# Performance work log

Measured on AMD Instinct MI355X. Metric: run time of the kernel, lower is better.

The kernel has to match this reference:

```python
import jax, jax.numpy as jnp
import numpy as np

B, L, D, N = 2, 8192, 1024, 512
EPS = 1e-5


def setup_inputs() -> dict:
    key = jax.random.key(0)
    ks = jax.random.split(key, 6)
    x = jax.random.normal(ks[0], (B, L, D), dtype=jnp.float32)
    Lambda_real = jax.random.normal(ks[1], (N,), dtype=jnp.float32)
    Lambda_imag = jax.random.normal(ks[2], (N,), dtype=jnp.float32)
    C_real = jax.random.normal(ks[3], (D, N), dtype=jnp.float32)
    C_imag = jax.random.normal(ks[4], (D, N), dtype=jnp.float32)
    param_D = jax.random.normal(ks[5], (D,), dtype=jnp.float32)
    gamma = jnp.ones((D,), dtype=jnp.float32)   # LayerNorm weight
    beta = jnp.zeros((D,), dtype=jnp.float32)   # LayerNorm bias
    return {"x": x, "Lambda_real": Lambda_real, "Lambda_imag": Lambda_imag,
            "C_real": C_real, "C_imag": C_imag, "param_D": param_D,
            "gamma": gamma, "beta": beta}


def reference(x, Lambda_real, Lambda_imag, C_real, C_imag, param_D, gamma, beta):
    seq_len = x.shape[1]
    # LayerNorm over last dim (biased variance, eps=1e-5, elementwise affine)
    mean = jnp.mean(x, axis=-1, keepdims=True)
    var = jnp.mean(jnp.square(x - mean), axis=-1, keepdims=True)
    u = (x - mean) * jax.lax.rsqrt(var + EPS) * gamma + beta   # [b, l, d]
    residual = u * param_D                                      # [b, l, d]
    # Diagonal SSM kernel synthesis
    Lam = -jnp.exp(Lambda_real) + 1j * jnp.exp(Lambda_imag)     # [n] complex
    C = (C_real + 1j * C_imag) * (jnp.exp(Lam) - 1.0) / Lam     # [d, n]
    ar = jnp.arange(seq_len, dtype=jnp.float32)
    S = jnp.exp(Lam[:, None] * ar[None, :])                     # [n, l] Vandermonde-like
    K = jnp.einsum('hn,nl->lh', C, S).real                      # [l, d]
    # FFT long convolution (linear conv via 2L zero-padding)
    n_fft = seq_len * 2
    u_f = jnp.fft.rfft(u, n=n_fft, axis=-2)                     # [b, l+1, d]
    K_f = jnp.fft.rfft(K, n=n_fft, axis=-2)                     # [l+1, d]
    y = jnp.fft.irfft(u_f * K_f, n=n_fft, axis=-2)[..., :seq_len, :]
    return y + residual
```

## Files before the change

### kernel.cpp

```cpp
#include <hip/hip_runtime.h>
#include <math.h>

#define LLEN 8192
#define DDIM 1024
#define NB   2
#define NMODE 512
#define MFFT 8192
#define SLEN 4096
#define KF_STRIDE 8208

#define PIDX(i) ((i) + ((i) >> 4))
#define FBUF 8704

#define OFF_UT   ((size_t)0)
#define OFF_KF   ((size_t)67108864)
#define OFF_KT   ((size_t)134348800)
#define OFF_CPK  ((size_t)167903232)
#define OFF_MEAN ((size_t)172097536)
#define OFF_RSTD ((size_t)172163072)
#define OFF_LAMR ((size_t)172228608)
#define OFF_LAMID ((size_t)172230656)
#define OFF_WR   ((size_t)172234752)
#define OFF_WI   ((size_t)172236800)
#define OFF_CUT  ((size_t)172238848)
#define OFF_TW   ((size_t)172240896)
#define OFF_TWR  ((size_t)172306432)
#define OFF_SORTN ((size_t)172371976)
#define OFF_TCNT  ((size_t)172374024)
#define WS_NEED  ((size_t)172374088)

#define OFF_SP   OFF_KF

__global__ __launch_bounds__(256) void ln_stats_kernel(const float* __restrict__ x,
                                                       float* __restrict__ mean,
                                                       float* __restrict__ rstd) {
  __shared__ float red[16];
  int row = blockIdx.x;
  int tid = threadIdx.x;
  const float4* xr = (const float4*)(x + (size_t)row * DDIM);
  float4 v = xr[tid];
  float s = v.x + v.y + v.z + v.w;
  float q = v.x*v.x + v.y*v.y + v.z*v.z + v.w*v.w;
  #pragma unroll
  for (int off = 32; off; off >>= 1) { s += __shfl_down(s, off); q += __shfl_down(q, off); }
  int wid = tid >> 6;
  if ((tid & 63) == 0) { red[wid] = s; red[8 + wid] = q; }
  __syncthreads();
  if (tid == 0) {
    float ts = red[0] + red[1] + red[2] + red[3];
    float tq = red[8] + red[9] + red[10] + red[11];
    float m = ts * (1.0f / DDIM);
    float var = tq * (1.0f / DDIM) - m * m;
    mean[row] = m;
    rstd[row] = rsqrtf(var + 1e-5f);
  }
}

__global__ __launch_bounds__(256) void transpose_ln_kernel(const float* __restrict__ x,
                                                           const float* __restrict__ mean,
                                                           const float* __restrict__ rstd,
                                                           const float* __restrict__ gamma,
                                                           const float* __restrict__ beta,
                                                           float* __restrict__ uT) {
  __shared__ float tile[32][33];
  int lt = blockIdx.x * 32, dt = blockIdx.y * 32, b = blockIdx.z;
  int c = threadIdx.x & 31, r0 = threadIdx.x >> 5;
  float gv = gamma[dt + c], bv = beta[dt + c];
  #pragma unroll
  for (int i = 0; i < 4; i++) {
    int r = r0 + i * 8;
    float m = mean[(size_t)b * LLEN + lt + r];
    float rs = rstd[(size_t)b * LLEN + lt + r];
    float xv = x[((size_t)b * LLEN + lt + r) * DDIM + dt + c];
    tile[r][c] = (xv - m) * rs * gv + bv;
  }
  __syncthreads();
  #pragma unroll
  for (int i = 0; i < 4; i++) {
    int r = r0 + i * 8;
    uT[((size_t)b * DDIM + dt + r) * LLEN + lt + c] = tile[c][r];
  }
}

__global__ void build_tables_kernel(const float* __restrict__ Lr, const float* __restrict__ Li,
                                    float* lamr, double* lamid, float* wre, float* wim, int* cut,
                                    float2* twH, float2* twR) {
  int gid = blockIdx.x * 256 + threadIdx.x;
  if (gid < NMODE) {
    double lr = (double)Lr[gid], li = (double)Li[gid];
    double ar = -exp(lr);
    double ai = exp(li);
    lamr[gid] = (float)ar;
    lamid[gid] = ai;
    double em = exp(ar);
    double cs = cos(ai), sn = sin(ai);
    double er = em * cs - 1.0;
    double ei = em * sn;
    double den = ar * ar + ai * ai;
    wre[gid] = (float)((er * ar + ei * ai) / den);
    wim[gid] = (float)((ei * ar - er * ai) / den);
    int co = (int)(40.0 / (-ar)) + 1;
    cut[gid] = co > SLEN ? SLEN : co;
  }
  int j = gid - NMODE;
  if (j >= 0 && j < 8192) {
    if (j == 0) {
      twH[0] = make_float2(1.f, 0.f);
    } else {
      int lev = 31 - __clz(j);
      int Ls = 1 << lev;
      int p = j - Ls;
      double a = 3.14159265358979323846264338 * (double)p / (double)Ls;
      twH[j] = make_float2((float)cos(a), (float)sin(a));
    }
  }
  int k = gid - (NMODE + 8192);
  if (k >= 0 && k <= 8192) {
    double a = 6.283185307179586476925287 * (double)k / 16384.0;
    twR[k] = make_float2((float)cos(a), (float)sin(a));
  }
}

#define KB4_LT 256
#define NTILE (SLEN / KB4_LT)
__global__ __launch_bounds__(NMODE) void sortmodes_kernel(const int* __restrict__ cut,
                                                          int* __restrict__ sortn,
                                                          int* __restrict__ tcount) {
  __shared__ int sc[NMODE];
  int tid = threadIdx.x;
  sc[tid] = cut[tid];
  __syncthreads();
  int c = sc[tid];
  int rank = 0;
  for (int m = 0; m < NMODE; ++m) {
    int cm = sc[m];
    rank += (cm > c) || (cm == c && m < tid);
  }
  sortn[rank] = tid;
  if (tid < NTILE) {
    int l0 = tid * KB4_LT;
    int cnt = 0;
    for (int m = 0; m < NMODE; ++m) cnt += (sc[m] > l0);
    tcount[tid] = cnt;
  }
}

__global__ __launch_bounds__(256) void cpack_kernel(const float* __restrict__ Cr,
                                                    const float* __restrict__ Ci,
                                                    const float* __restrict__ wre,
                                                    const float* __restrict__ wim,
                                                    const int* __restrict__ sortn,
                                                    float2* __restrict__ Cpk) {
  int idx = blockIdx.x * 256 + threadIdx.x;
  int r = idx >> 10, d = idx & (DDIM - 1);
  int n = sortn[r];
  float cr = Cr[(size_t)d * NMODE + n], ci = Ci[(size_t)d * NMODE + n];
  float wr = wre[n], wi = wim[n];
  Cpk[idx] = make_float2(cr * wr - ci * wi, cr * wi + ci * wr);
}

__global__ __launch_bounds__(256) void sbuild_kernel(const float* __restrict__ lamr,
                                                     const double* __restrict__ lamid,
                                                     const int* __restrict__ cut,
                                                     const int* __restrict__ sortn,
                                                     float2* __restrict__ Spack) {
  int r = blockIdx.y;
  int n = sortn[r];
  int l = blockIdx.x * 256 + threadIdx.x;
  float sr = 0.f, si = 0.f;
  if (l < cut[n]) {
    float mag = expf(lamr[n] * (float)l);
    double ph = lamid[n] * (double)l;
    const double tp = 6.283185307179586476925287;
    const double itp = 1.0 / 6.283185307179586476925287;
    ph -= floor(ph * itp) * tp;
    float cs, sn; sincosf((float)ph, &sn, &cs);
    sr = mag * cs; si = mag * sn;
  }
  Spack[(size_t)r * SLEN + l] = make_float2(sr, si);
}

#define KB5_DT 4
__global__ __launch_bounds__(256) void kbuild7_kernel(const float2* __restrict__ Spack,
                                                      const float2* __restrict__ Cpk,
                                                      const int* __restrict__ tcount,
                                                      float* __restrict__ KT) {
  __shared__ float2 sC[NMODE][KB5_DT];
  int t = blockIdx.y;
  int d0 = blockIdx.x * KB5_DT;
  int tid = threadIdx.x;
  int nact = tcount[t];
  for (int i = tid; i < nact * KB5_DT; i += 256) {
    int r = i >> 2, dd = i & 3;
    sC[r][dd] = Cpk[(size_t)r * DDIM + d0 + dd];
  }
  __syncthreads();
  int l = t * KB4_LT + tid;
  float acc0 = 0.f, acc1 = 0.f, acc2 = 0.f, acc3 = 0.f;
  const float2* sp = Spack + l;
  int i = 0;
  int n8 = nact & ~7;
  for (; i < n8; i += 8) {
    const float2* p = sp + (size_t)i * SLEN;
    float2 s0 = p[0];
    float2 s1 = p[(size_t)1 * SLEN];
    float2 s2 = p[(size_t)2 * SLEN];
    float2 s3 = p[(size_t)3 * SLEN];
    float2 s4 = p[(size_t)4 * SLEN];
    float2 s5 = p[(size_t)5 * SLEN];
    float2 s6 = p[(size_t)6 * SLEN];
    float2 s7 = p[(size_t)7 * SLEN];
    #define KACC(ss, rr) { \
      float2 c0 = sC[rr][0], c1 = sC[rr][1], c2 = sC[rr][2], c3 = sC[rr][3]; \
      acc0 += ss.x * c0.x - ss.y * c0.y; \
      acc1 += ss.x * c1.x - ss.y * c1.y; \
      acc2 += ss.x * c2.x - ss.y * c2.y; \
      acc3 += ss.x * c3.x - ss.y * c3.y; }
    KACC(s0, i + 0) KACC(s1, i + 1) KACC(s2, i + 2) KACC(s3, i + 3)
    KACC(s4, i + 4) KACC(s5, i + 5) KACC(s6, i + 6) KACC(s7, i + 7)
  }
  for (; i < nact; ++i) {
    float2 s0 = sp[(size_t)i * SLEN];
    KACC(s0, i)
  }
  #undef KACC
  KT[(size_t)(d0 + 0) * SLEN + l] = acc0;
  KT[(size_t)(d0 + 1) * SLEN + l] = acc1;
  KT[(size_t)(d0 + 2) * SLEN + l] = acc2;
  KT[(size_t)(d0 + 3) * SLEN + l] = acc3;
}

#define R4BLK(b0, b2, b1, b3, wa, wb, o0, o1, o2, o3) { \
  float war=(wa).x, wai=sign*(wa).y, wbr=(wb).x, wbi=sign*(wb).y; \
  float t1r_=war*(b2).x - wai*(b2).y, t1i_=war*(b2).y + wai*(b2).x; \
  float t3r_=war*(b3).x - wai*(b3).y, t3i_=war*(b3).y + wai*(b3).x; \
  float Ar=(b0).x+t1r_, Ai=(b0).y+t1i_, Cr=(b0).x-t1r_, Ci=(b0).y-t1i_; \
  float Br=(b1).x+t3r_, Bi=(b1).y+t3i_, Dr=(b1).x-t3r_, Di=(b1).y-t3i_; \
  float Er=wbr*Br-wbi*Bi, Ei=wbr*Bi+wbi*Br; \
  float Fr=wbr*Dr-wbi*Di, Fi=wbr*Di+wbi*Dr; \
  dst[PIDX(o0)]=make_float2(Ar+Er,Ai+Ei); \
  dst[PIDX(o1)]=make_float2(Cr-sign*Fi,Ci+sign*Fr); \
  dst[PIDX(o2)]=make_float2(Ar-Er,Ai-Ei); \
  dst[PIDX(o3)]=make_float2(Cr+sign*Fi,Ci-sign*Fr); }

__device__ __forceinline__ void r8_stage(const float2* src, float2* dst,
                                         const float2* __restrict__ twH,
                                         int tid, float sign, int s) {
  int L = 1 << s;
  int j = tid;
  int p = j & (L - 1);
  int q = j >> s;
  float2 x0 = src[PIDX(j)];
  float2 x1 = src[PIDX(j + 1024)];
  float2 x2 = src[PIDX(j + 2048)];
  float2 x3 = src[PIDX(j + 3072)];
  float2 x4 = src[PIDX(j + 4096)];
  float2 x5 = src[PIDX(j + 5120)];
  float2 x6 = src[PIDX(j + 6144)];
  float2 x7 = src[PIDX(j + 7168)];
  float2 w1 = twH[L + p];
  float w1r = w1.x, w1i = sign * w1.y;
  float t4r = w1r*x4.x - w1i*x4.y, t4i = w1r*x4.y + w1i*x4.x;
  float t5r = w1r*x5.x - w1i*x5.y, t5i = w1r*x5.y + w1i*x5.x;
  float t6r = w1r*x6.x - w1i*x6.y, t6i = w1r*x6.y + w1i*x6.x;
  float t7r = w1r*x7.x - w1i*x7.y, t7i = w1r*x7.y + w1i*x7.x;
  float2 A0 = make_float2(x0.x + t4r, x0.y + t4i), B0 = make_float2(x0.x - t4r, x0.y - t4i);
  float2 A1 = make_float2(x1.x + t5r, x1.y + t5i), B1 = make_float2(x1.x - t5r, x1.y - t5i);
  float2 A2 = make_float2(x2.x + t6r, x2.y + t6i), B2 = make_float2(x2.x - t6r, x2.y - t6i);
  float2 A3 = make_float2(x3.x + t7r, x3.y + t7i), B3 = make_float2(x3.x - t7r, x3.y - t7i);
  int O = (q << (s + 3)) + p;
  R4BLK(A0, A2, A1, A3, twH[2*L + p], twH[4*L + p], O, O + 2*L, O + 4*L, O + 6*L)
  R4BLK(B0, B2, B1, B3, twH[3*L + p], twH[5*L + p], O + L, O + 3*L, O + 5*L, O + 7*L)
}

__device__ __forceinline__ void r8_first4(const float2* __restrict__ g, float2* dst,
                                          const float2* __restrict__ twH,
                                          int tid, float sign) {
  float2 x0 = g[tid];
  float2 x1 = g[tid + 1024];
  float2 x2 = g[tid + 2048];
  float2 x3 = g[tid + 3072];
  int O = tid << 3;
  R4BLK(x0, x2, x1, x3, twH[2], twH[4], O, O + 2, O + 4, O + 6)
  R4BLK(x0, x2, x1, x3, twH[3], twH[5], O + 1, O + 3, O + 5, O + 7)
}

__device__ __forceinline__ void r8_first2(const float2* __restrict__ g, float2* dst,
                                          const float2* __restrict__ twH,
                                          int tid, float sign) {
  float2 x0 = g[tid];
  float2 x1 = g[tid + 1024];
  float2 zf = make_float2(0.f, 0.f);
  int O = tid << 3;
  R4BLK(x0, zf, x1, zf, twH[2], twH[4], O, O + 2, O + 4, O + 6)
  R4BLK(x0, zf, x1, zf, twH[3], twH[5], O + 1, O + 3, O + 5, O + 7)
}

__device__ __forceinline__ void fwd_final_pair(const float2* sbuf, const float2* __restrict__ twH,
                                               int k, float2* zk, float2* zm) {
  float2 a1 = sbuf[PIDX(k)], b1 = sbuf[PIDX(k + 4096)];
  float2 w1 = twH[4096 + k];
  float br1 = w1.x*b1.x + w1.y*b1.y;
  float bi1 = w1.x*b1.y - w1.y*b1.x;
  *zk = make_float2(a1.x + br1, a1.y + bi1);
  float2 a2 = sbuf[PIDX(4096 - k)], b2 = sbuf[PIDX(8192 - k)];
  float2 w2 = twH[8192 - k];
  float br2 = w2.x*b2.x + w2.y*b2.y;
  float bi2 = w2.x*b2.y - w2.y*b2.x;
  *zm = make_float2(a2.x - br2, a2.y - bi2);
}

__global__ __launch_bounds__(1024) void kf_fft_kernel(const float* __restrict__ KT,
                                                      const float2* __restrict__ twH,
                                                      const float2* __restrict__ twR,
                                                      float2* __restrict__ Kf) {
  __shared__ float2 bufA[FBUF];
  __shared__ float2 bufB[FBUF];
  int d = blockIdx.x;
  int tid = threadIdx.x;
  const float2* row = (const float2*)(KT + (size_t)d * SLEN);
  const float sign = -1.f;
  { float2* dst = bufA; r8_first2(row, dst, twH, tid, sign); }
  __syncthreads();
  r8_stage(bufA, bufB, twH, tid, sign, 3);
  __syncthreads();
  r8_stage(bufB, bufA, twH, tid, sign, 6);
  __syncthreads();
  r8_stage(bufA, bufB, twH, tid, sign, 9);
  __syncthreads();
  const float scale = 1.0f / 8192.0f;
  float2* out = Kf + (size_t)d * KF_STRIDE;
  for (int k = tid; k <= 4096; k += 1024) {
    if (k == 0) {
      float2 s0 = bufB[PIDX(0)], s4 = bufB[PIDX(4096)];
      float2 z0 = make_float2(s0.x + s4.x, s0.y + s4.y);
      out[0]    = make_float2((z0.x + z0.y) * scale, 0.f);
      out[8192] = make_float2((z0.x - z0.y) * scale, 0.f);
    } else {
      float2 zk, zm;
      if (k == 4096) {
        float2 s0 = bufB[PIDX(0)], s4 = bufB[PIDX(4096)];
        zk = make_float2(s0.x - s4.x, s0.y - s4.y);
        zm = zk;
      } else {
        fwd_final_pair(bufB, twH, k, &zk, &zm);
      }
      float Ar = 0.5f * (zk.x + zm.x), Ai = 0.5f * (zk.y - zm.y);
      float Br = 0.5f * (zk.x - zm.x), Bi = 0.5f * (zk.y + zm.y);
      float2 t = twR[k];
      float c = t.x, sn = t.y;
      float e1r = sn * Br - c * Bi;
      float e1i = sn * Bi + c * Br;
      out[k]        = make_float2((Ar - e1r) * scale, (Ai - e1i) * scale);
      out[MFFT - k] = make_float2((Ar + e1r) * scale, (-Ai - e1i) * scale);
    }
  }
}

__global__ __launch_bounds__(1024) void conv_fft_kernel(float* __restrict__ uT,
                                                        const float2* __restrict__ twH,
                                                        const float2* __restrict__ twR,
                                                        const float2* __restrict__ Kf,
                                                        const float* __restrict__ pD) {
  __shared__ float2 bufA[FBUF];
  __shared__ float2 bufB[FBUF];
  int wg = blockIdx.x;
  int b = wg >> 10, d = wg & (DDIM - 1);
  int tid = threadIdx.x;
  float2* row = (float2*)(uT + ((size_t)b * DDIM + d) * LLEN);
  float sign = -1.f;
  { float2* dst = bufA; r8_first4(row, dst, twH, tid, sign); }
  __syncthreads();
  r8_stage(bufA, bufB, twH, tid, sign, 3);
  __syncthreads();
  r8_stage(bufB, bufA, twH, tid, sign, 6);
  __syncthreads();
  r8_stage(bufA, bufB, twH, tid, sign, 9);
  __syncthreads();
  const float2* kf = Kf + (size_t)d * KF_STRIDE;
  for (int k = tid; k <= 4096; k += 1024) {
    if (k == 0) {
      float2 s0 = bufB[PIDX(0)], s4 = bufB[PIDX(4096)];
      float2 z0 = make_float2(s0.x + s4.x, s0.y + s4.y);
      float U0 = z0.x + z0.y;
      float UM = z0.x - z0.y;
      float Y0 = U0 * kf[0].x;
      float YM = UM * kf[8192].x;
      bufA[PIDX(0)] = make_float2(0.5f * (Y0 + YM), 0.5f * (Y0 - YM));
    } else {
      float2 zk, zm;
      if (k == 4096) {
        float2 s0 = bufB[PIDX(0)], s4 = bufB[PIDX(4096)];
        zk = make_float2(s0.x - s4.x, s0.y - s4.y);
        zm = zk;
      } else {
        fwd_final_pair(bufB, twH, k, &zk, &zm);
      }
      float Ar = 0.5f * (zk.x + zm.x), Ai = 0.5f * (zk.y - zm.y);
      float Br = 0.5f * (zk.x - zm.x), Bi = 0.5f * (zk.y + zm.y);
      float2 t = twR[k];
      float c = t.x, sn = t.y;
      float e1r = sn * Br - c * Bi;
      float e1i = sn * Bi + c * Br;
      float Ukr = Ar - e1r, Uki = Ai - e1i;
      float Umr = Ar + e1r, Umi = -Ai - e1i;
      float2 kk = kf[k], km = kf[MFFT - k];
      float Ykr = Ukr * kk.x - Uki * kk.y, Yki = Ukr * kk.y + Uki * kk.x;
      float Ymr = Umr * km.x - Umi * km.y, Ymi = Umr * km.y + Umi * km.x;
      float Eyr = 0.5f * (Ykr + Ymr), Eyi = 0.5f * (Yki - Ymi);
      float Byr = 0.5f * (Ykr - Ymr), Byi = 0.5f * (Yki + Byi*0.f + Yki*0.f + Ymi);
      Byi = 0.5f * (Yki + Ymi);
      bufA[PIDX(k)]        = make_float2(Eyr - sn * Byr - c * Byi, Eyi + c * Byr - sn * Byi);
      bufA[PIDX(MFFT - k)] = make_float2(Eyr + sn * Byr + c * Byi, -Eyi + c * Byr - sn * Byi);
    }
  }
  __syncthreads();
  sign = +1.f;
  r8_stage(bufA, bufB, twH, tid, sign, 0);
  __syncthreads();
  r8_stage(bufB, bufA, twH, tid, sign, 3);
  __syncthreads();
  r8_stage(bufA, bufB, twH, tid, sign, 6);
  __syncthreads();
  r8_stage(bufB, bufA, twH, tid, sign, 9);
  __syncthreads();
  float pdv = pD[d];
  for (int j = tid; j < 4096; j += 1024) {
    float2 a = bufA[PIDX(j)];
    float2 bq = bufA[PIDX(j + 4096)];
    float2 w = twH[4096 + j];
    float br = w.x * bq.x - w.y * bq.y;
    float bi = w.x * bq.y + w.y * bq.x;
    float2 uv = row[j];
    row[j] = make_float2(a.x + br + uv.x * pdv, a.y + bi + uv.y * pdv);
  }
}

__global__ __launch_bounds__(256) void final_kernel(const float* __restrict__ yT,
                                                    float* __restrict__ out) {
  __shared__ float tile[32][33];
  int lt = blockIdx.x * 32, dt = blockIdx.y * 32, b = blockIdx.z;
  int c = threadIdx.x & 31, r0 = threadIdx.x >> 5;
  #pragma unroll
  for (int i = 0; i < 4; i++) {
    int r = r0 + i * 8;
    tile[r][c] = yT[((size_t)b * DDIM + dt + r) * LLEN + lt + c];
  }
  __syncthreads();
  #pragma unroll
  for (int i = 0; i < 4; i++) {
    int r = r0 + i * 8;
    out[((size_t)b * LLEN + lt + r) * DDIM + dt + c] = tile[c][r];
  }
}

extern "C" void kernel_launch(void* const* d_in, const int* in_sizes, int n_in,
                              void* d_out, int out_size, void* d_ws, size_t ws_size,
                              hipStream_t stream) {
  (void)in_sizes; (void)n_in; (void)out_size;
  if (ws_size < WS_NEED) return;
  const float* x     = (const float*)d_in[0];
  const float* Lr    = (const float*)d_in[1];
  const float* Li    = (const float*)d_in[2];
  const float* Cr    = (const float*)d_in[3];
  const float* Ci    = (const float*)d_in[4];
  const float* pD    = (const float*)d_in[5];
  const float* gamma = (const float*)d_in[6];
  const float* beta  = (const float*)d_in[7];
  float* out = (float*)d_out;
  char* ws = (char*)d_ws;

  float*  UT    = (float*)(ws + OFF_UT);
  float2* KF    = (float2*)(ws + OFF_KF);
  float2* SPK   = (float2*)(ws + OFF_SP);
  float*  KT    = (float*)(ws + OFF_KT);
  float2* CPK   = (float2*)(ws + OFF_CPK);
  float*  MEAN  = (float*)(ws + OFF_MEAN);
  float*  RSTD  = (float*)(ws + OFF_RSTD);
  float*  LAMR  = (float*)(ws + OFF_LAMR);
  double* LAMID = (double*)(ws + OFF_LAMID);
  float*  WRe   = (float*)(ws + OFF_WR);
  float*  WIm   = (float*)(ws + OFF_WI);
  int*    CUT   = (int*)(ws + OFF_CUT);
  float2* TWH   = (float2*)(ws + OFF_TW);
  float2* TWR   = (float2*)(ws + OFF_TWR);
  int*    SORTN = (int*)(ws + OFF_SORTN);
  int*    TCNT  = (int*)(ws + OFF_TCNT);

  ln_stats_kernel<<<NB * LLEN, 256, 0, stream>>>(x, MEAN, RSTD);
  transpose_ln_kernel<<<dim3(LLEN / 32, DDIM / 32, NB), 256, 0, stream>>>(x, MEAN, RSTD, gamma, beta, UT);
  build_tables_kernel<<<67, 256, 0, stream>>>(Lr, Li, LAMR, LAMID, WRe, WIm, CUT, TWH, TWR);
  sortmodes_kernel<<<1, NMODE, 0, stream>>>(CUT, SORTN, TCNT);
  cpack_kernel<<<(NMODE * DDIM) / 256, 256, 0, stream>>>(Cr, Ci, WRe, WIm, SORTN, CPK);
  sbuild_kernel<<<dim3(SLEN / 256, NMODE), 256, 0, stream>>>(LAMR, LAMID, CUT, SORTN, SPK);
  kbuild7_kernel<<<dim3(DDIM / KB5_DT, NTILE), 256, 0, stream>>>(SPK, CPK, TCNT, KT);
  kf_fft_kernel<<<DDIM, 1024, 0, stream>>>(KT, TWH, TWR, KF);
  conv_fft_kernel<<<NB * DDIM, 1024, 0, stream>>>(UT, TWH, TWR, KF, pD);
  final_kernel<<<dim3(LLEN / 32, DDIM / 32, NB), 256, 0, stream>>>(UT, out);
}
```

Before: 299.4 us.

## Make FFT stages in-place to halve LDS and allow two blocks per CU

Replaces the ping-pong shared buffers in the FFT kernels with a single buffer, putting a barrier between the loads and stores of each radix-8 stage. The pointwise spectrum multiply is also restructured so each thread computes its symmetric pairs in registers before writing back in place. This halves LDS use per block (about 70KB down to 35KB), so more 1024-thread blocks can be resident per CU, at the cost of an extra barrier per stage and more register pressure.

```diff
diff --git a/kernel.cpp b/kernel.cpp
--- a/kernel.cpp
+++ b/kernel.cpp
@@ -243,21 +243,20 @@
   dst[PIDX(o2)]=make_float2(Ar-Er,Ai-Ei); \
   dst[PIDX(o3)]=make_float2(Cr+sign*Fi,Ci-sign*Fr); }
 
-__device__ __forceinline__ void r8_stage(const float2* src, float2* dst,
-                                         const float2* __restrict__ twH,
-                                         int tid, float sign, int s) {
+__device__ __forceinline__ void r8_stage_ip(float2* buf, const float2* __restrict__ twH,
+                                            int tid, float sign, int s) {
   int L = 1 << s;
   int j = tid;
   int p = j & (L - 1);
   int q = j >> s;
-  float2 x0 = src[PIDX(j)];
-  float2 x1 = src[PIDX(j + 1024)];
-  float2 x2 = src[PIDX(j + 2048)];
-  float2 x3 = src[PIDX(j + 3072)];
-  float2 x4 = src[PIDX(j + 4096)];
-  float2 x5 = src[PIDX(j + 5120)];
-  float2 x6 = src[PIDX(j + 6144)];
-  float2 x7 = src[PIDX(j + 7168)];
+  float2 x0 = buf[PIDX(j)];
+  float2 x1 = buf[PIDX(j + 1024)];
+  float2 x2 = buf[PIDX(j + 2048)];
+  float2 x3 = buf[PIDX(j + 3072)];
+  float2 x4 = buf[PIDX(j + 4096)];
+  float2 x5 = buf[PIDX(j + 5120)];
+  float2 x6 = buf[PIDX(j + 6144)];
+  float2 x7 = buf[PIDX(j + 7168)];
   float2 w1 = twH[L + p];
   float w1r = w1.x, w1i = sign * w1.y;
   float t4r = w1r*x4.x - w1i*x4.y, t4i = w1r*x4.y + w1i*x4.x;
@@ -268,32 +267,11 @@
   float2 A1 = make_float2(x1.x + t5r, x1.y + t5i), B1 = make_float2(x1.x - t5r, x1.y - t5i);
   float2 A2 = make_float2(x2.x + t6r, x2.y + t6i), B2 = make_float2(x2.x - t6r, x2.y - t6i);
   float2 A3 = make_float2(x3.x + t7r, x3.y + t7i), B3 = make_float2(x3.x - t7r, x3.y - t7i);
+  __syncthreads();
+  float2* dst = buf;
   int O = (q << (s + 3)) + p;
   R4BLK(A0, A2, A1, A3, twH[2*L + p], twH[4*L + p], O, O + 2*L, O + 4*L, O + 6*L)
   R4BLK(B0, B2, B1, B3, twH[3*L + p], twH[5*L + p], O + L, O + 3*L, O + 5*L, O + 7*L)
-}
-
-__device__ __forceinline__ void r8_first4(const float2* __restrict__ g, float2* dst,
-                                          const float2* __restrict__ twH,
-                                          int tid, float sign) {
-  float2 x0 = g[tid];
-  float2 x1 = g[tid + 1024];
-  float2 x2 = g[tid + 2048];
-  float2 x3 = g[tid + 3072];
-  int O = tid << 3;
-  R4BLK(x0, x2, x1, x3, twH[2], twH[4], O, O + 2, O + 4, O + 6)
-  R4BLK(x0, x2, x1, x3, twH[3], twH[5], O + 1, O + 3, O + 5, O + 7)
-}
-
-__device__ __forceinline__ void r8_first2(const float2* __restrict__ g, float2* dst,
-                                          const float2* __restrict__ twH,
-                                          int tid, float sign) {
-  float2 x0 = g[tid];
-  float2 x1 = g[tid + 1024];
-  float2 zf = make_float2(0.f, 0.f);
-  int O = tid << 3;
-  R4BLK(x0, zf, x1, zf, twH[2], twH[4], O, O + 2, O + 4, O + 6)
-  R4BLK(x0, zf, x1, zf, twH[3], twH[5], O + 1, O + 3, O + 5, O + 7)
 }
 
 __device__ __forceinline__ void fwd_final_pair(const float2* sbuf, const float2* __restrict__ twH,
@@ -310,40 +288,77 @@
   *zm = make_float2(a2.x - br2, a2.y - bi2);
 }
 
-__global__ __launch_bounds__(1024) void kf_fft_kernel(const float* __restrict__ KT,
-                                                      const float2* __restrict__ twH,
-                                                      const float2* __restrict__ twR,
-                                                      float2* __restrict__ Kf) {
-  __shared__ float2 bufA[FBUF];
-  __shared__ float2 bufB[FBUF];
+__device__ __forceinline__ void pw_pair(float2 zk, float2 zm, int k,
+                                        const float2* __restrict__ twR,
+                                        const float2* __restrict__ kf,
+                                        float2* outk, float2* outm) {
+  float Ar = 0.5f * (zk.x + zm.x), Ai = 0.5f * (zk.y - zm.y);
+  float Br = 0.5f * (zk.x - zm.x), Bi = 0.5f * (zk.y + zm.y);
+  float2 t = twR[k];
+  float c = t.x, sn = t.y;
+  float e1r = sn * Br - c * Bi;
+  float e1i = sn * Bi + c * Br;
+  float Ukr = Ar - e1r, Uki = Ai - e1i;
+  float Umr = Ar + e1r, Umi = -Ai - e1i;
+  float2 kk = kf[k], km = kf[MFFT - k];
+  float Ykr = Ukr * kk.x - Uki * kk.y, Yki = Ukr * kk.y + Uki * kk.x;
+  float Ymr = Umr * km.x - Umi * km.y, Ymi = Umr * km.y + Umi * km.x;
+  float Eyr = 0.5f * (Ykr + Ymr), Eyi = 0.5f * (Yki - Ymi);
+  float Byr = 0.5f * (Ykr - Ymr), Byi = 0.5f * (Yki + Ymi);
+  *outk = make_float2(Eyr - sn * Byr - c * Byi, Eyi + c * Byr - sn * Byi);
+  *outm = make_float2(Eyr + sn * Byr + c * Byi, -Eyi + c * Byr - sn * Byi);
+}
+
+__device__ __forceinline__ void pw_compute(const float2* buf, const float2* __restrict__ twH,
+                                           const float2* __restrict__ twR,
+                                           const float2* __restrict__ kf,
+                                           int k, float2* outk, float2* outm) {
+  float2 zk, zm;
+  fwd_final_pair(buf, twH, k, &zk, &zm);
+  pw_pair(zk, zm, k, twR, kf, outk, outm);
+}
+
+__global__ __launch_bounds__(1024, 8) void kf_fft_kernel(const float* __restrict__ KT,
+                                                         const float2* __restrict__ twH,
+                                                         const float2* __restrict__ twR,
+                                                         float2* __restrict__ Kf) {
+  __shared__ float2 buf[FBUF];
   int d = blockIdx.x;
   int tid = threadIdx.x;
   const float2* row = (const float2*)(KT + (size_t)d * SLEN);
   const float sign = -1.f;
-  { float2* dst = bufA; r8_first2(row, dst, twH, tid, sign); }
-  __syncthreads();
-  r8_stage(bufA, bufB, twH, tid, sign, 3);
-  __syncthreads();
-  r8_stage(bufB, bufA, twH, tid, sign, 6);
-  __syncthreads();
-  r8_stage(bufA, bufB, twH, tid, sign, 9);
+  {
+    float2* dst = buf;
+    float2 x0 = row[tid];
+    float2 x1 = row[tid + 1024];
+    float2 zf = make_float2(0.f, 0.f);
+    int O = tid << 3;
+    R4BLK(x0, zf, x1, zf, twH[2], twH[4], O, O + 2, O + 4, O + 6)
+    R4BLK(x0, zf, x1, zf, twH[3], twH[5], O + 1, O + 3, O + 5, O + 7)
+  }
+  __syncthreads();
+  r8_stage_ip(buf, twH, tid, sign, 3);
+  __syncthreads();
+  r8_stage_ip(buf, twH, tid, sign, 6);
+  __syncthreads();
+  r8_stage_ip(buf, twH, tid, sign, 9);
   __syncthreads();
   const float scale = 1.0f / 8192.0f;
   float2* out = Kf + (size_t)d * KF_STRIDE;
   for (int k = tid; k <= 4096; k += 1024) {
     if (k == 0) {
-      float2 s0 = bufB[PIDX(0)], s4 = bufB[PIDX(4096)];
+      float2 s0 = buf[PIDX(0)], s4 = buf[PIDX(4096)];
       float2 z0 = make_float2(s0.x + s4.x, s0.y + s4.y);
       out[0]    = make_float2((z0.x + z0.y) * scale, 0.f);
       out[8192] = make_float2((z0.x - z0.y) * scale, 0.f);
     } else {
       float2 zk, zm;
       if (k == 4096) {
-        float2 s0 = bufB[PIDX(0)], s4 = bufB[PIDX(4096)];
+        float2 s0 = buf[PIDX(0)], s4 = buf[PIDX(4096)];
         zk = make_float2(s0.x - s4.x, s0.y - s4.y);
         zm = zk;
       } else {
-        fwd_final_pair(bufB, twH, k, &zk, &zm);
+        fwd_final_pair(buf, twH, k, &zk, &zm);
       }
       float Ar = 0.5f * (zk.x + zm.x), Ai = 0.5f * (zk.y - zm.y);
       float Br = 0.5f * (zk.x - zm.x), Bi = 0.5f * (zk.y + zm.y);
@@ -357,77 +372,89 @@
   }
 }
 
-__global__ __launch_bounds__(1024) void conv_fft_kernel(float* __restrict__ uT,
-                                                        const float2* __restrict__ twH,
-                                                        const float2* __restrict__ twR,
-                                                        const float2* __restrict__ Kf,
-                                                        const float* __restrict__ pD) {
-  __shared__ float2 bufA[FBUF];
-  __shared__ float2 bufB[FBUF];
+__global__ __launch_bounds__(1024, 8) void conv_fft_kernel(float* __restrict__ uT,
+                                                           const float2* __restrict__ twH,
+                                                           const float2* __restrict__ twR,
+                                                           const float2* __restrict__ Kf,
+                                                           const float* __restrict__ pD) {
+  __shared__ float2 buf[FBUF];
   int wg = blockIdx.x;
   int b = wg >> 10, d = wg & (DDIM - 1);
   int tid = threadIdx.x;
   float2* row = (float2*)(uT + ((size_t)b * DDIM + d) * LLEN);
   float sign = -1.f;
-  { float2* dst = bufA; r8_first4(row, dst, twH, tid, sign); }
-  __syncthreads();
-  r8_stage(bufA, bufB, twH, tid, sign, 3);
-  __syncthreads();
-  r8_stage(bufB, bufA, twH, tid, sign, 6);
-  __syncthreads();
-  r8_stage(bufA, bufB, twH, tid, sign, 9);
+  {
+    float2* dst = buf;
+    float2 x0 = row[tid];
+    float2 x1 = row[tid + 1024];
+    float2 x2 = row[tid + 2048];
+    float2 x3 = row[tid + 3072];
+    int O = tid << 3;
+    R4BLK(x0, x2, x1, x3, twH[2], twH[4], O, O + 2, O + 4, O + 6)
+    R4BLK(x0, x2, x1, x3, twH[3], twH[5], O + 1, O + 3, O + 5, O + 7)
+  }
+  __syncthreads();
+  r8_stage_ip(buf, twH, tid, sign, 3);
+  __syncthreads();
+  r8_stage_ip(buf, twH, tid, sign, 6);
+  __syncthreads();
+  r8_stage_ip(buf, twH, tid, sign, 9);
   __syncthreads();
   const float2* kf = Kf + (size_t)d * KF_STRIDE;
-  for (int k = tid; k <= 4096; k += 1024) {
-    if (k == 0) {
-      float2 s0 = bufB[PIDX(0)], s4 = bufB[PIDX(4096)];
+  {
+    float2 oA0, oA1, oB0, oB1;
+    if (tid == 0) {
+      float2 s0 = buf[PIDX(0)], s4 = buf[PIDX(4096)];
       float2 z0 = make_float2(s0.x + s4.x, s0.y + s4.y);
       float U0 = z0.x + z0.y;
       float UM = z0.x - z0.y;
       float Y0 = U0 * kf[0].x;
       float YM = UM * kf[8192].x;
-      bufA[PIDX(0)] = make_float2(0.5f * (Y0 + YM), 0.5f * (Y0 - YM));
+      oA0 = make_float2(0.5f * (Y0 + YM), 0.5f * (Y0 - YM));
+      float2 zk = make_float2(s0.x - s4.x, s0.y - s4.y);
+      float2 dum;
+      pw_pair(zk, zk, 4096, twR, kf, &oB0, &dum);
+      oA1 = oB1 = make_float2(0.f, 0.f);
     } else {
-      float2 zk, zm;
-      if (k == 4096) {
-        float2 s0 = bufB[PIDX(0)], s4 = bufB[PIDX(4096)];
-        zk = make_float2(s0.x - s4.x, s0.y - s4.y);
-        zm = zk;
-      } else {
-        fwd_final_pair(bufB, twH, k, &zk, &zm);
-      }
-      float Ar = 0.5f * (zk.x + zm.x), Ai = 0.5f * (zk.y - zm.y);
-      float Br = 0.5f * (zk.x - zm.x), Bi = 0.5f * (zk.y + zm.y);
-      float2 t = twR[k];
-      float c = t.x, sn = t.y;
-      float e1r = sn * Br - c * Bi;
-      float e1i = sn * Bi + c * Br;
-      float Ukr = Ar - e1r, Uki = Ai - e1i;
-      float Umr = Ar + e1r, Umi = -Ai - e1i;
-      float2 kk = kf[k], km = kf[MFFT - k];
-      float Ykr = Ukr * kk.x - Uki * kk.y, Yki = Ukr * kk.y + Uki * kk.x;
-      float Ymr = Umr * km.x - Umi * km.y, Ymi = Umr * km.y + Umi * km.x;
-      float Eyr = 0.5f * (Ykr + Ymr), Eyi = 0.5f * (Yki - Ymi);
-      float Byr = 0.5f * (Ykr - Ymr), Byi = 0.5f * (Yki + Byi*0.f + Yki*0.f + Ymi);
-      Byi = 0.5f * (Yki + Ymi);
-      bufA[PIDX(k)]        = make_float2(Eyr - sn * Byr - c * Byi, Eyi + c * Byr - sn * Byi);
-      bufA[PIDX(MFFT - k)] = make_float2(Eyr + sn * Byr + c * Byi, -Eyi + c * Byr - sn * Byi);
+      pw_compute(buf, twH, twR, kf, tid, &oA0, &oA1);
+      pw_compute(buf, twH, twR, kf, 4096 - tid, &oB0, &oB1);
     }
-  }
-  __syncthreads();
+    __syncthreads();
+    if (tid == 0) {
+      buf[PIDX(0)] = oA0;
+      buf[PIDX(4096)] = oB0;
+    } else {
+      buf[PIDX(tid)] = oA0;        buf[PIDX(8192 - tid)] = oA1;
+      buf[PIDX(4096 - tid)] = oB0; buf[PIDX(4096 + tid)] = oB1;
+    }
+    __syncthreads();
+  }
+  {
+    float2 oC0, oC1, oD0, oD1, oE0, oE1;
+    int kC = 1024 + tid;
+    int kD = 3072 - tid;
+    pw_compute(buf, twH, twR, kf, kC, &oC0, &oC1);
+    pw_compute(buf, twH, twR, kf, kD, &oD0, &oD1);
+    if (tid == 0) pw_compute(buf, twH, twR, kf, 2048, &oE0, &oE1);
+    __syncthreads();
+    buf[PIDX(kC)] = oC0; buf[PIDX(8192 - kC)] = oC1;
+    buf[PIDX(kD)] = oD0; buf[PIDX(8192 - kD)] = oD1;
+    if (tid == 0) { buf[PIDX(2048)] = oE0; buf[PIDX(6144)] = oE1; }
+    __syncthreads();
+  }
   sign = +1.f;
-  r8_stage(bufA, bufB, twH, tid, sign, 0);
-  __syncthreads();
-  r8_stage(bufB, bufA, twH, tid, sign, 3);
-  __syncthreads();
-  r8_stage(bufA, bufB, twH, tid, sign, 6);
-  __syncthreads();
-  r8_stage(bufB, bufA, twH, tid, sign, 9);
+  r8_stage_ip(buf, twH, tid, sign, 0);
+  __syncthreads();
+  r8_stage_ip(buf, twH, tid, sign, 3);
+  __syncthreads();
+  r8_stage_ip(buf, twH, tid, sign, 6);
+  __syncthreads();
+  r8_stage_ip(buf, twH, tid, sign, 9);
   __syncthreads();
   float pdv = pD[d];
   for (int j = tid; j < 4096; j += 1024) {
-    float2 a = bufA[PIDX(j)];
-    float2 bq = bufA[PIDX(j + 4096)];
+    float2 a = buf[PIDX(j)];
+    float2 bq = buf[PIDX(j + 4096)];
     float2 w = twH[4096 + j];
     float br = w.x * bq.x - w.y * bq.y;
     float bi = w.x * bq.y + w.y * bq.x;
```

After: 317.0 us. 5.9% more time.
